# Kernel tuning notes

Hardware: AMD Instinct MI355X
Metric: run time of the kernel (lower is better)

The kernel has to match this reference:

```python
import jax, jax.numpy as jnp
import numpy as np

EPS = 1e-5
C_M, C, C_Z = 256, 32, 128
N_SEQ, N_RES = 256, 1024


def setup_inputs() -> dict:
    key = jax.random.key(0)
    k1, k2, k3 = jax.random.split(key, 3)
    msa = jax.random.normal(k1, (N_SEQ, N_RES, C_M), dtype=jnp.float32)
    norm_w = jnp.ones((C_M,), dtype=jnp.float32)
    norm_b = jnp.zeros((C_M,), dtype=jnp.float32)
    w_ab = jax.random.normal(k2, (C, C_M), dtype=jnp.float32) * (1.0 / np.sqrt(C_M))
    b_ab = jnp.zeros((C,), dtype=jnp.float32)
    w_out = jax.random.normal(k3, (C_Z, C * C), dtype=jnp.float32) * (1.0 / C)
    b_out = jnp.zeros((C_Z,), dtype=jnp.float32)
    return {"msa": msa, "norm_w": norm_w, "norm_b": norm_b,
            "w_ab": w_ab, "b_ab": b_ab, "w_out": w_out, "b_out": b_out}


def reference(msa, norm_w, norm_b, w_ab, b_ab, w_out, b_out):
    # msa: (s, r, c_m) -> (r, s, c_m)
    x = jnp.transpose(msa, (1, 0, 2))
    s = x.shape[1]
    # LayerNorm over c_m
    mu = jnp.mean(x, axis=-1, keepdims=True)
    var = jnp.mean(jnp.square(x - mu), axis=-1, keepdims=True)
    xn = (x - mu) * jax.lax.rsqrt(var + EPS) * norm_w + norm_b
    # a == b: same linear applied twice to same input in the original
    a = jnp.einsum('rsm,cm->rsc', xn, w_ab) + b_ab          # (r, s, c)
    # mean over s of outer product == batched A^T A / s  -> (r, c, c)
    o = jnp.einsum('rsx,rsy->rxy', a, a) / s
    o = o.reshape(o.shape[0], C * C)                        # (r, c*c)
    pre_pair = jnp.einsum('rk,zk->rz', o, w_out) + b_out    # (r, c_z)
    r = pre_pair.shape[0]
    # unsqueeze(1).expand(r, r, c_z)
    pair = jnp.broadcast_to(pre_pair[:, None, :], (r, r, C_Z))
    return pair
```

## Files before the change

kernel.cpp:

```cpp
#include <hip/hip_runtime.h>

#define NSEQ 256
#define NRES 1024
#define CM   256
#define CC   32
#define CZ   128
#define EPS  1e-5f
#define SROW (NRES * CM)
#define MCH  32
#define XPAD 36

typedef float f4v __attribute__((ext_vector_type(4)));

__global__ void opm_setup(const float* __restrict__ nw,
                          const float* __restrict__ nb,
                          const float* __restrict__ w_ab,
                          const float* __restrict__ b_ab,
                          float* __restrict__ wt_g,
                          float* __restrict__ k12)
{
    __shared__ float wls[CM * CC];
    const int t = threadIdx.x;
    const float nwm = nw[t];
    #pragma unroll
    for (int c = 0; c < CC; ++c)
        wls[t * CC + c] = nwm * w_ab[c * CM + t];
    __syncthreads();
    for (int i = t; i < CM * CC; i += 256) wt_g[i] = wls[i];
    if (t < CC) {
        float k1 = 0.f, k2 = 0.f;
        for (int m = 0; m < CM; ++m) {
            k1 += wls[m * CC + t];
            k2 = fmaf(nb[m], w_ab[t * CM + m], k2);
        }
        k12[t]      = k1;
        k12[CC + t] = k2 + b_ab[t];
    }
}

__launch_bounds__(256, 3)
__global__ void opm_compute(const float* __restrict__ msa,
                            const float* __restrict__ wt_g,
                            const float* __restrict__ k12,
                            const float* __restrict__ w_out,
                            const float* __restrict__ b_out,
                            float* __restrict__ pre_out)
{
    __shared__ float xt[NSEQ * XPAD];
    __shared__ float o_lds[CC * CC];
    __shared__ float mu_s[NSEQ];
    __shared__ float rs_s[NSEQ];
    __shared__ float pre_part[2 * CZ];

    const int tid  = threadIdx.x;
    const int r    = blockIdx.x;
    const int lane = tid & 63;
    const int wave = tid >> 6;
    const int cw   = __builtin_amdgcn_readfirstlane(wave << 3);

    const int sc = tid & 7;
    const int sg = tid >> 3;
    const float* xr = msa + (size_t)r * CM;

    float G[4][8];
    #pragma unroll
    for (int j = 0; j < 4; ++j)
        #pragma unroll
        for (int c = 0; c < 8; ++c) G[j][c] = 0.f;

    float psum[8], pssq[8];
    #pragma unroll
    for (int k = 0; k < 8; ++k) { psum[k] = 0.f; pssq[k] = 0.f; }

    float4 pf[8];
    #pragma unroll
    for (int k = 0; k < 8; ++k)
        pf[k] = *(const float4*)(xr + (size_t)(sg + (k << 5)) * SROW + (sc << 2));

    for (int mb = 0; mb < CM; mb += MCH) {
        __syncthreads();
        #pragma unroll
        for (int k = 0; k < 8; ++k) {
            *(float4*)&xt[(sg + (k << 5)) * XPAD + (sc << 2)] = pf[k];
            psum[k] += (pf[k].x + pf[k].y) + (pf[k].z + pf[k].w);
            pssq[k]  = fmaf(pf[k].x, pf[k].x, fmaf(pf[k].y, pf[k].y,
                       fmaf(pf[k].z, pf[k].z, fmaf(pf[k].w, pf[k].w, pssq[k]))));
        }
        __syncthreads();
        if (mb + MCH < CM) {
            #pragma unroll
            for (int k = 0; k < 8; ++k)
                pf[k] = *(const float4*)(xr + (size_t)(sg + (k << 5)) * SROW + (mb + MCH) + (sc << 2));
        }
        #pragma unroll
        for (int mm = 0; mm < MCH; mm += 4) {
            const float4 x0 = *(const float4*)&xt[(lane      ) * XPAD + mm];
            const float4 x1 = *(const float4*)&xt[(lane +  64) * XPAD + mm];
            const float4 x2 = *(const float4*)&xt[(lane + 128) * XPAD + mm];
            const float4 x3 = *(const float4*)&xt[(lane + 192) * XPAD + mm];
            const float* wr = wt_g + (((mb + mm) << 5) + cw);
            #pragma unroll
            for (int kk = 0; kk < 4; ++kk) {
                float wv[8];
                #pragma unroll
                for (int c = 0; c < 8; ++c) wv[c] = wr[(kk << 5) + c];
                const float a0 = (kk == 0) ? x0.x : (kk == 1) ? x0.y : (kk == 2) ? x0.z : x0.w;
                const float a1 = (kk == 0) ? x1.x : (kk == 1) ? x1.y : (kk == 2) ? x1.z : x1.w;
                const float a2 = (kk == 0) ? x2.x : (kk == 1) ? x2.y : (kk == 2) ? x2.z : x2.w;
                const float a3 = (kk == 0) ? x3.x : (kk == 1) ? x3.y : (kk == 2) ? x3.z : x3.w;
                #pragma unroll
                for (int c = 0; c < 8; ++c) {
                    G[0][c] = fmaf(a0, wv[c], G[0][c]);
                    G[1][c] = fmaf(a1, wv[c], G[1][c]);
                    G[2][c] = fmaf(a2, wv[c], G[2][c]);
                    G[3][c] = fmaf(a3, wv[c], G[3][c]);
                }
            }
        }
    }

    #pragma unroll
    for (int k = 0; k < 8; ++k) {
        float s1 = psum[k], s2 = pssq[k];
        s1 += __shfl_xor(s1, 1); s1 += __shfl_xor(s1, 2); s1 += __shfl_xor(s1, 4);
        s2 += __shfl_xor(s2, 1); s2 += __shfl_xor(s2, 2); s2 += __shfl_xor(s2, 4);
        if (sc == 0) {
            const float mu  = s1 * (1.f / CM);
            const float var = s2 * (1.f / CM) - mu * mu;
            mu_s[sg + (k << 5)] = mu;
            rs_s[sg + (k << 5)] = 1.f / sqrtf(var + EPS);
        }
    }
    __syncthreads();

    {
        float k1v[8], k2v[8];
        #pragma unroll
        for (int c = 0; c < 8; ++c) { k1v[c] = k12[cw + c]; k2v[c] = k12[CC + cw + c]; }
        #pragma unroll
        for (int j = 0; j < 4; ++j) {
            const int s = lane + (j << 6);
            const float mu = mu_s[s], rstd = rs_s[s];
            float av[8];
            #pragma unroll
            for (int c = 0; c < 8; ++c)
                av[c] = fmaf(rstd, G[j][c] - mu * k1v[c], k2v[c]);
            const int sw = s & 7;
            *(float4*)&xt[s * CC + ((((wave << 1)    ) ^ sw) << 2)] =
                make_float4(av[0], av[1], av[2], av[3]);
            *(float4*)&xt[s * CC + ((((wave << 1) | 1) ^ sw) << 2)] =
                make_float4(av[4], av[5], av[6], av[7]);
        }
    }
    __syncthreads();

    const int grp = wave;
    const int xs  = (tid >> 3) & 7;
    const int ys  = tid & 7;
    float4 pr0 = {0,0,0,0}, pr1 = {0,0,0,0}, pr2 = {0,0,0,0}, pr3 = {0,0,0,0};
    #pragma unroll 4
    for (int si = 0; si < 64; ++si) {
        const int s  = (grp << 6) + si;
        const int sw = si & 7;
        const float4 ax = *(const float4*)&xt[s * CC + ((xs ^ sw) << 2)];
        const float4 ay = *(const float4*)&xt[s * CC + ((ys ^ sw) << 2)];
        pr0.x = fmaf(ax.x, ay.x, pr0.x); pr0.y = fmaf(ax.x, ay.y, pr0.y);
        pr0.z = fmaf(ax.x, ay.z, pr0.z); pr0.w = fmaf(ax.x, ay.w, pr0.w);
        pr1.x = fmaf(ax.y, ay.x, pr1.x); pr1.y = fmaf(ax.y, ay.y, pr1.y);
        pr1.z = fmaf(ax.y, ay.z, pr1.z); pr1.w = fmaf(ax.y, ay.w, pr1.w);
        pr2.x = fmaf(ax.z, ay.x, pr2.x); pr2.y = fmaf(ax.z, ay.y, pr2.y);
        pr2.z = fmaf(ax.z, ay.z, pr2.z); pr2.w = fmaf(ax.z, ay.w, pr2.w);
        pr3.x = fmaf(ax.w, ay.x, pr3.x); pr3.y = fmaf(ax.w, ay.y, pr3.y);
        pr3.z = fmaf(ax.w, ay.z, pr3.z); pr3.w = fmaf(ax.w, ay.w, pr3.w);
    }
    __syncthreads();
    {
        float* pb = &xt[(grp << 10) + ((xs << 2) * CC) + (ys << 2)];
        *(float4*)&pb[0 * CC] = pr0;
        *(float4*)&pb[1 * CC] = pr1;
        *(float4*)&pb[2 * CC] = pr2;
        *(float4*)&pb[3 * CC] = pr3;
    }
    __syncthreads();
    {
        const float inv_s = 1.f / NSEQ;
        float4 acc = *(const float4*)&xt[(tid << 2)];
        const float4 b1 = *(const float4*)&xt[1024 + (tid << 2)];
        const float4 b2 = *(const float4*)&xt[2048 + (tid << 2)];
        const float4 b3 = *(const float4*)&xt[3072 + (tid << 2)];
        acc.x = (acc.x + b1.x + b2.x + b3.x) * inv_s;
        acc.y = (acc.y + b1.y + b2.y + b3.y) * inv_s;
        acc.z = (acc.z + b1.z + b2.z + b3.z) * inv_s;
        acc.w = (acc.w + b1.w + b2.w + b3.w) * inv_s;
        *(float4*)&o_lds[tid << 2] = acc;
    }
    __syncthreads();

    {
        const int z    = tid & 127;
        const int half = tid >> 7;
        const float* wrow = w_out + (size_t)z * (CC * CC) + half * 512;
        const float* op   = o_lds + half * 512;
        float po = 0.f;
        #pragma unroll 8
        for (int k = 0; k < 512; k += 4) {
            const float4 o4 = *(const float4*)&op[k];
            const float4 w4 = *(const float4*)&wrow[k];
            po = fmaf(o4.x, w4.x, fmaf(o4.y, w4.y, fmaf(o4.z, w4.z, fmaf(o4.w, w4.w, po))));
        }
        pre_part[half * CZ + z] = po;
    }
    __syncthreads();
    if (tid < CZ)
        pre_out[(size_t)r * CZ + tid] = pre_part[tid] + pre_part[CZ + tid] + b_out[tid];
}

__launch_bounds__(256, 8)
__global__ void opm_bcast(const float* __restrict__ pre,
                          float* __restrict__ out)
{
    const int bid = blockIdx.x;
    const int r   = bid >> 3;
    const int jb  = bid & 7;
    const int z4  = threadIdx.x & 31;
    const int jo  = threadIdx.x >> 5;

    const f4v pv = *((const f4v*)(pre + (size_t)r * CZ) + z4);
    f4v* outp = (f4v*)out + ((size_t)r * NRES + (size_t)jb * 128) * (CZ / 4);
    for (int j0 = 0; j0 < 128; j0 += 8)
        __builtin_nontemporal_store(pv, &outp[(size_t)(j0 + jo) * (CZ / 4) + z4]);
}

extern "C" void kernel_launch(void* const* d_in, const int* in_sizes, int n_in,
                              void* d_out, int out_size, void* d_ws, size_t ws_size,
                              hipStream_t stream) {
    const float* msa   = (const float*)d_in[0];
    const float* nw    = (const float*)d_in[1];
    const float* nb    = (const float*)d_in[2];
    const float* w_ab  = (const float*)d_in[3];
    const float* b_ab  = (const float*)d_in[4];
    const float* w_out = (const float*)d_in[5];
    const float* b_out = (const float*)d_in[6];
    float* out = (float*)d_out;

    float* pre  = (float*)d_ws;
    float* wt_g = pre + (size_t)NRES * CZ;
    float* k12  = wt_g + CM * CC;

    opm_setup<<<1, 256, 0, stream>>>(nw, nb, w_ab, b_ab, wt_g, k12);
    opm_compute<<<NRES, 256, 0, stream>>>(msa, wt_g, k12, w_out, b_out, pre);
    opm_bcast<<<NRES * 8, 256, 0, stream>>>(pre, out);
}
```

Measured before the change: 822.2 us.

## Stage projection weights in LDS and remap per-thread tile for LN-projection GEMM

The folded projection weights are copied once per block into shared memory instead of being read from global memory inside the inner loop. The thread tile changes from 4 sequences by 8 channels to 8 sequences by 4 channels, with float4 weight loads from LDS. The msa staging chunk shrinks from 32 to 16 columns, and the smaller buffers are aliased into the existing arrays to keep LDS usage down. The trade-off is 32KB of extra LDS per block, which may lower occupancy, and twice as many chunk iterations and barriers.

```diff
diff --git a/kernel.cpp b/kernel.cpp
--- a/kernel.cpp
+++ b/kernel.cpp
@@ -7,8 +7,8 @@
 #define CZ   128
 #define EPS  1e-5f
 #define SROW (NRES * CM)
-#define MCH  32
-#define XPAD 36
+#define MCH  16
+#define XPAD 20
 
 typedef float f4v __attribute__((ext_vector_type(4)));
 
@@ -46,42 +46,46 @@
                             const float* __restrict__ b_out,
                             float* __restrict__ pre_out)
 {
+    __shared__ float wt[CM * CC];
     __shared__ float xt[NSEQ * XPAD];
-    __shared__ float o_lds[CC * CC];
-    __shared__ float mu_s[NSEQ];
-    __shared__ float rs_s[NSEQ];
-    __shared__ float pre_part[2 * CZ];
 
     const int tid  = threadIdx.x;
     const int r    = blockIdx.x;
-    const int lane = tid & 63;
     const int wave = tid >> 6;
-    const int cw   = __builtin_amdgcn_readfirstlane(wave << 3);
-
-    const int sc = tid & 7;
-    const int sg = tid >> 3;
+
+    const int sc4 = tid & 3;
+    const int sg4 = tid >> 2;
+    const int sc8 = tid & 7;
+    const int sg8 = tid >> 3;
+    const int c0  = sc8 << 2;
+
     const float* xr = msa + (size_t)r * CM;
 
-    float G[4][8];
-    #pragma unroll
-    for (int j = 0; j < 4; ++j)
-        #pragma unroll
-        for (int c = 0; c < 8; ++c) G[j][c] = 0.f;
-
-    float psum[8], pssq[8];
-    #pragma unroll
-    for (int k = 0; k < 8; ++k) { psum[k] = 0.f; pssq[k] = 0.f; }
-
-    float4 pf[8];
-    #pragma unroll
-    for (int k = 0; k < 8; ++k)
-        pf[k] = *(const float4*)(xr + (size_t)(sg + (k << 5)) * SROW + (sc << 2));
+    float4 pf[4];
+    #pragma unroll
+    for (int k = 0; k < 4; ++k)
+        pf[k] = *(const float4*)(xr + (size_t)(sg4 + (k << 6)) * SROW + (sc4 << 2));
+
+    #pragma unroll
+    for (int k = 0; k < 8; ++k) {
+        const int i = (tid + (k << 8)) << 2;
+        *(float4*)&wt[i] = *(const float4*)&wt_g[i];
+    }
+
+    float G[8][4];
+    #pragma unroll
+    for (int j = 0; j < 8; ++j) {
+        G[j][0] = 0.f; G[j][1] = 0.f; G[j][2] = 0.f; G[j][3] = 0.f;
+    }
+    float psum[4], pssq[4];
+    #pragma unroll
+    for (int k = 0; k < 4; ++k) { psum[k] = 0.f; pssq[k] = 0.f; }
 
     for (int mb = 0; mb < CM; mb += MCH) {
         __syncthreads();
         #pragma unroll
-        for (int k = 0; k < 8; ++k) {
-            *(float4*)&xt[(sg + (k << 5)) * XPAD + (sc << 2)] = pf[k];
+        for (int k = 0; k < 4; ++k) {
+            *(float4*)&xt[(sg4 + (k << 6)) * XPAD + (sc4 << 2)] = pf[k];
             psum[k] += (pf[k].x + pf[k].y) + (pf[k].z + pf[k].w);
             pssq[k]  = fmaf(pf[k].x, pf[k].x, fmaf(pf[k].y, pf[k].y,
                        fmaf(pf[k].z, pf[k].z, fmaf(pf[k].w, pf[k].w, pssq[k]))));
@@ -89,67 +93,55 @@
         __syncthreads();
         if (mb + MCH < CM) {
             #pragma unroll
-            for (int k = 0; k < 8; ++k)
-                pf[k] = *(const float4*)(xr + (size_t)(sg + (k << 5)) * SROW + (mb + MCH) + (sc << 2));
+            for (int k = 0; k < 4; ++k)
+                pf[k] = *(const float4*)(xr + (size_t)(sg4 + (k << 6)) * SROW + (mb + MCH) + (sc4 << 2));
         }
         #pragma unroll
         for (int mm = 0; mm < MCH; mm += 4) {
-            const float4 x0 = *(const float4*)&xt[(lane      ) * XPAD + mm];
-            const float4 x1 = *(const float4*)&xt[(lane +  64) * XPAD + mm];
-            const float4 x2 = *(const float4*)&xt[(lane + 128) * XPAD + mm];
-            const float4 x3 = *(const float4*)&xt[(lane + 192) * XPAD + mm];
-            const float* wr = wt_g + (((mb + mm) << 5) + cw);
+            const float4 w0 = *(const float4*)&wt[(mb + mm + 0) * CC + c0];
+            const float4 w1 = *(const float4*)&wt[(mb + mm + 1) * CC + c0];
+            const float4 w2 = *(const float4*)&wt[(mb + mm + 2) * CC + c0];
+            const float4 w3 = *(const float4*)&wt[(mb + mm + 3) * CC + c0];
             #pragma unroll
-            for (int kk = 0; kk < 4; ++kk) {
-                float wv[8];
-                #pragma unroll
-                for (int c = 0; c < 8; ++c) wv[c] = wr[(kk << 5) + c];
-                const float a0 = (kk == 0) ? x0.x : (kk == 1) ? x0.y : (kk == 2) ? x0.z : x0.w;
-                const float a1 = (kk == 0) ? x1.x : (kk == 1) ? x1.y : (kk == 2) ? x1.z : x1.w;
-                const float a2 = (kk == 0) ? x2.x : (kk == 1) ? x2.y : (kk == 2) ? x2.z : x2.w;
-                const float a3 = (kk == 0) ? x3.x : (kk == 1) ? x3.y : (kk == 2) ? x3.z : x3.w;
-                #pragma unroll
-                for (int c = 0; c < 8; ++c) {
-                    G[0][c] = fmaf(a0, wv[c], G[0][c]);
-                    G[1][c] = fmaf(a1, wv[c], G[1][c]);
-                    G[2][c] = fmaf(a2, wv[c], G[2][c]);
-                    G[3][c] = fmaf(a3, wv[c], G[3][c]);
-                }
+            for (int j = 0; j < 8; ++j) {
+                const float4 x4 = *(const float4*)&xt[(sg8 + (j << 5)) * XPAD + mm];
+                G[j][0] = fmaf(x4.x, w0.x, fmaf(x4.y, w1.x, fmaf(x4.z, w2.x, fmaf(x4.w, w3.x, G[j][0]))));
+                G[j][1] = fmaf(x4.x, w0.y, fmaf(x4.y, w1.y, fmaf(x4.z, w2.y, fmaf(x4.w, w3.y, G[j][1]))));
+                G[j][2] = fmaf(x4.x, w0.z, fmaf(x4.y, w1.z, fmaf(x4.z, w2.z, fmaf(x4.w, w3.z, G[j][2]))));
+                G[j][3] = fmaf(x4.x, w0.w, fmaf(x4.y, w1.w, fmaf(x4.z, w2.w, fmaf(x4.w, w3.w, G[j][3]))));
             }
         }
     }
-
-    #pragma unroll
-    for (int k = 0; k < 8; ++k) {
+    __syncthreads();
+
+    #pragma unroll
+    for (int k = 0; k < 4; ++k) {
         float s1 = psum[k], s2 = pssq[k];
-        s1 += __shfl_xor(s1, 1); s1 += __shfl_xor(s1, 2); s1 += __shfl_xor(s1, 4);
-        s2 += __shfl_xor(s2, 1); s2 += __shfl_xor(s2, 2); s2 += __shfl_xor(s2, 4);
-        if (sc == 0) {
+        s1 += __shfl_xor(s1, 1); s1 += __shfl_xor(s1, 2);
+        s2 += __shfl_xor(s2, 1); s2 += __shfl_xor(s2, 2);
+        if (sc4 == 0) {
+            const int s = sg4 + (k << 6);
             const float mu  = s1 * (1.f / CM);
             const float var = s2 * (1.f / CM) - mu * mu;
-            mu_s[sg + (k << 5)] = mu;
-            rs_s[sg + (k << 5)] = 1.f / sqrtf(var + EPS);
-        }
-    }
-    __syncthreads();
-
-    {
-        float k1v[8], k2v[8];
+            xt[s]        = mu;
+            xt[NSEQ + s] = 1.f / sqrtf(var + EPS);
+        }
+    }
+    __syncthreads();
+
+    {
+        const float4 k1v = *(const float4*)&k12[c0];
+        const float4 k2v = *(const float4*)&k12[CC + c0];
         #pragma unroll
-        for (int c = 0; c < 8; ++c) { k1v[c] = k12[cw + c]; k2v[c] = k12[CC + cw + c]; }
-        #pragma unroll
-        for (int j = 0; j < 4; ++j) {
-            const int s = lane + (j << 6);
-            const float mu = mu_s[s], rstd = rs_s[s];
-            float av[8];
-            #pragma unroll
-            for (int c = 0; c < 8; ++c)
-                av[c] = fmaf(rstd, G[j][c] - mu * k1v[c], k2v[c]);
-            const int sw = s & 7;
-            *(float4*)&xt[s * CC + ((((wave << 1)    ) ^ sw) << 2)] =
-                make_float4(av[0], av[1], av[2], av[3]);
-            *(float4*)&xt[s * CC + ((((wave << 1) | 1) ^ sw) << 2)] =
-                make_float4(av[4], av[5], av[6], av[7]);
+        for (int j = 0; j < 8; ++j) {
+            const int s = sg8 + (j << 5);
+            const float mu = xt[s], rstd = xt[NSEQ + s];
+            float4 av;
+            av.x = fmaf(rstd, G[j][0] - mu * k1v.x, k2v.x);
+            av.y = fmaf(rstd, G[j][1] - mu * k1v.y, k2v.y);
+            av.z = fmaf(rstd, G[j][2] - mu * k1v.z, k2v.z);
+            av.w = fmaf(rstd, G[j][3] - mu * k1v.w, k2v.w);
+            *(float4*)&wt[s * CC + ((sc8 ^ (s & 7)) << 2)] = av;
         }
     }
     __syncthreads();
@@ -162,8 +154,8 @@
     for (int si = 0; si < 64; ++si) {
         const int s  = (grp << 6) + si;
         const int sw = si & 7;
-        const float4 ax = *(const float4*)&xt[s * CC + ((xs ^ sw) << 2)];
-        const float4 ay = *(const float4*)&xt[s * CC + ((ys ^ sw) << 2)];
+        const float4 ax = *(const float4*)&wt[s * CC + ((xs ^ sw) << 2)];
+        const float4 ay = *(const float4*)&wt[s * CC + ((ys ^ sw) << 2)];
         pr0.x = fmaf(ax.x, ay.x, pr0.x); pr0.y = fmaf(ax.x, ay.y, pr0.y);
         pr0.z = fmaf(ax.x, ay.z, pr0.z); pr0.w = fmaf(ax.x, ay.w, pr0.w);
         pr1.x = fmaf(ax.y, ay.x, pr1.x); pr1.y = fmaf(ax.y, ay.y, pr1.y);
@@ -173,13 +165,12 @@
         pr3.x = fmaf(ax.w, ay.x, pr3.x); pr3.y = fmaf(ax.w, ay.y, pr3.y);
         pr3.z = fmaf(ax.w, ay.z, pr3.z); pr3.w = fmaf(ax.w, ay.w, pr3.w);
     }
-    __syncthreads();
-    {
-        float* pb = &xt[(grp << 10) + ((xs << 2) * CC) + (ys << 2)];
-        *(float4*)&pb[0 * CC] = pr0;
-        *(float4*)&pb[1 * CC] = pr1;
-        *(float4*)&pb[2 * CC] = pr2;
-        *(float4*)&pb[3 * CC] = pr3;
+    {
+        float* pb = &xt[(grp << 10) + (xs << 7) + (ys << 2)];
+        *(float4*)&pb[0 << 5] = pr0;
+        *(float4*)&pb[1 << 5] = pr1;
+        *(float4*)&pb[2 << 5] = pr2;
+        *(float4*)&pb[3 << 5] = pr3;
     }
     __syncthreads();
     {
@@ -192,7 +183,7 @@
         acc.y = (acc.y + b1.y + b2.y + b3.y) * inv_s;
         acc.z = (acc.z + b1.z + b2.z + b3.z) * inv_s;
         acc.w = (acc.w + b1.w + b2.w + b3.w) * inv_s;
-        *(float4*)&o_lds[tid << 2] = acc;
+        *(float4*)&xt[tid << 2] = acc;
     }
     __syncthreads();
 
@@ -200,7 +191,7 @@
         const int z    = tid & 127;
         const int half = tid >> 7;
         const float* wrow = w_out + (size_t)z * (CC * CC) + half * 512;
-        const float* op   = o_lds + half * 512;
+        const float* op   = &xt[half * 512];
         float po = 0.f;
         #pragma unroll 8
         for (int k = 0; k < 512; k += 4) {
@@ -208,11 +199,11 @@
             const float4 w4 = *(const float4*)&wrow[k];
             po = fmaf(o4.x, w4.x, fmaf(o4.y, w4.y, fmaf(o4.z, w4.z, fmaf(o4.w, w4.w, po))));
         }
-        pre_part[half * CZ + z] = po;
+        xt[4096 + (half << 7) + z] = po;
     }
     __syncthreads();
     if (tid < CZ)
-        pre_out[(size_t)r * CZ + tid] = pre_part[tid] + pre_part[CZ + tid] + b_out[tid];
+        pre_out[(size_t)r * CZ + tid] = xt[4096 + tid] + xt[4096 + CZ + tid] + b_out[tid];
 }
 
 __launch_bounds__(256, 8)
```

After: 795.4 us. 1.03x faster.

## Use split-bf16 MFMA for LayerNorm-projection GEMM instead of scalar FP32 FMAs

Applied to the files above, without the earlier changes.

Replaces the scalar FP32 FMA loop computing x·W (256 seq × 256 ch × 32 out per residue) with bf16 MFMA 16x16x32 instructions. Precision is kept by splitting both x and W into high and low bf16 parts and summing three cross products. Weights are pre-split and pre-swizzled into MFMA fragment layout in the setup kernel and staged in LDS. LDS use grows, so launch bounds drop to 2 blocks per CU. The approach risks small numerical error from dropping the low×low term.

```diff
diff --git a/kernel.cpp b/kernel.cpp
--- a/kernel.cpp
+++ b/kernel.cpp
@@ -7,17 +7,25 @@
 #define CZ   128
 #define EPS  1e-5f
 #define SROW (NRES * CM)
-#define MCH  32
-#define XPAD 36
 
 typedef float f4v __attribute__((ext_vector_type(4)));
+typedef __attribute__((ext_vector_type(8))) short short8;
+typedef __attribute__((ext_vector_type(4))) float f32x4;
+typedef unsigned int u32;
+
+__device__ __forceinline__ float trunc_bf16(float f) {
+    return __uint_as_float(__float_as_uint(f) & 0xffff0000u);
+}
+__device__ __forceinline__ u32 pk_bf16(float a, float b) {
+    return (__float_as_uint(b) & 0xffff0000u) | (__float_as_uint(a) >> 16);
+}
 
 __global__ void opm_setup(const float* __restrict__ nw,
                           const float* __restrict__ nb,
                           const float* __restrict__ w_ab,
                           const float* __restrict__ b_ab,
-                          float* __restrict__ wt_g,
-                          float* __restrict__ k12)
+                          float* __restrict__ k12,
+                          unsigned short* __restrict__ wb_su)
 {
     __shared__ float wls[CM * CC];
     const int t = threadIdx.x;
@@ -26,7 +34,6 @@
     for (int c = 0; c < CC; ++c)
         wls[t * CC + c] = nwm * w_ab[c * CM + t];
     __syncthreads();
-    for (int i = t; i < CM * CC; i += 256) wt_g[i] = wls[i];
     if (t < CC) {
         float k1 = 0.f, k2 = 0.f;
         for (int m = 0; m < CM; ++m) {
@@ -36,38 +43,54 @@
         k12[t]      = k1;
         k12[CC + t] = k2 + b_ab[t];
     }
-}
-
-__launch_bounds__(256, 3)
+    for (int e = t; e < 16384; e += 256) {
+        const int j     = e & 7;
+        const int l     = (e >> 3) & 63;
+        const int split = (e >> 9) & 1;
+        const int nt    = (e >> 10) & 1;
+        const int kk    = e >> 11;
+        const int m = (kk << 5) + ((l >> 4) << 3) + j;
+        const int c = (nt << 4) + (l & 15);
+        const float w  = wls[m * CC + c];
+        const float w1 = trunc_bf16(w);
+        const float v  = split ? (w - w1) : w;
+        wb_su[e] = (unsigned short)(__float_as_uint(v) >> 16);
+    }
+}
+
+__launch_bounds__(256, 2)
 __global__ void opm_compute(const float* __restrict__ msa,
-                            const float* __restrict__ wt_g,
+                            const u32*  __restrict__ wb_g,
                             const float* __restrict__ k12,
                             const float* __restrict__ w_out,
                             const float* __restrict__ b_out,
                             float* __restrict__ pre_out)
 {
-    __shared__ float xt[NSEQ * XPAD];
-    __shared__ float o_lds[CC * CC];
-    __shared__ float mu_s[NSEQ];
-    __shared__ float rs_s[NSEQ];
-    __shared__ float pre_part[2 * CZ];
-
-    const int tid  = threadIdx.x;
-    const int r    = blockIdx.x;
-    const int lane = tid & 63;
-    const int wave = tid >> 6;
-    const int cw   = __builtin_amdgcn_readfirstlane(wave << 3);
-
-    const int sc = tid & 7;
-    const int sg = tid >> 3;
-    const float* xr = msa + (size_t)r * CM;
-
-    float G[4][8];
-    #pragma unroll
-    for (int j = 0; j < 4; ++j)
-        #pragma unroll
-        for (int c = 0; c < 8; ++c) G[j][c] = 0.f;
-
+    __shared__ u32 xp[2 * 5120];
+    __shared__ u32 wbl[8192];
+    __shared__ float st[520];
+
+    const int tid = threadIdx.x;
+    const int r   = blockIdx.x;
+    const int w   = tid >> 6;
+    const int l   = tid & 63;
+
+    const int sc8 = tid & 7;
+    const int sg8 = tid >> 3;
+    const float* xr = msa + (size_t)r * CM + (sc8 << 2);
+
+    u32* xp1 = xp;
+    u32* xp2 = xp + 5120;
+
+    #pragma unroll
+    for (int k = 0; k < 8; ++k) {
+        const int i = (tid + (k << 8)) << 2;
+        *(f4v*)&wbl[i] = *(const f4v*)&wb_g[i];
+    }
+
+    f32x4 acc[4][2];
+    #pragma unroll
+    for (int mt = 0; mt < 4; ++mt) { acc[mt][0] = (f32x4)0.f; acc[mt][1] = (f32x4)0.f; }
     float psum[8], pssq[8];
     #pragma unroll
     for (int k = 0; k < 8; ++k) { psum[k] = 0.f; pssq[k] = 0.f; }
@@ -75,95 +98,101 @@
     float4 pf[8];
     #pragma unroll
     for (int k = 0; k < 8; ++k)
-        pf[k] = *(const float4*)(xr + (size_t)(sg + (k << 5)) * SROW + (sc << 2));
-
-    for (int mb = 0; mb < CM; mb += MCH) {
+        pf[k] = *(const float4*)(xr + (size_t)(sg8 + (k << 5)) * SROW);
+
+    for (int kk = 0; kk < 8; ++kk) {
         __syncthreads();
         #pragma unroll
         for (int k = 0; k < 8; ++k) {
-            *(float4*)&xt[(sg + (k << 5)) * XPAD + (sc << 2)] = pf[k];
-            psum[k] += (pf[k].x + pf[k].y) + (pf[k].z + pf[k].w);
-            pssq[k]  = fmaf(pf[k].x, pf[k].x, fmaf(pf[k].y, pf[k].y,
-                       fmaf(pf[k].z, pf[k].z, fmaf(pf[k].w, pf[k].w, pssq[k]))));
+            const float4 p = pf[k];
+            const int row = sg8 + (k << 5);
+            const u32 a0 = pk_bf16(p.x, p.y), a1 = pk_bf16(p.z, p.w);
+            const float rx = p.x - trunc_bf16(p.x);
+            const float ry = p.y - trunc_bf16(p.y);
+            const float rz = p.z - trunc_bf16(p.z);
+            const float rw = p.w - trunc_bf16(p.w);
+            const u32 b0 = pk_bf16(rx, ry), b1 = pk_bf16(rz, rw);
+            *(uint2*)&xp1[row * 20 + (sc8 << 1)] = make_uint2(a0, a1);
+            *(uint2*)&xp2[row * 20 + (sc8 << 1)] = make_uint2(b0, b1);
+            psum[k] += (p.x + p.y) + (p.z + p.w);
+            pssq[k]  = fmaf(p.x, p.x, fmaf(p.y, p.y, fmaf(p.z, p.z, fmaf(p.w, p.w, pssq[k]))));
         }
         __syncthreads();
-        if (mb + MCH < CM) {
+        if (kk < 7) {
             #pragma unroll
             for (int k = 0; k < 8; ++k)
-                pf[k] = *(const float4*)(xr + (size_t)(sg + (k << 5)) * SROW + (mb + MCH) + (sc << 2));
-        }
-        #pragma unroll
-        for (int mm = 0; mm < MCH; mm += 4) {
-            const float4 x0 = *(const float4*)&xt[(lane      ) * XPAD + mm];
-            const float4 x1 = *(const float4*)&xt[(lane +  64) * XPAD + mm];
-            const float4 x2 = *(const float4*)&xt[(lane + 128) * XPAD + mm];
-            const float4 x3 = *(const float4*)&xt[(lane + 192) * XPAD + mm];
-            const float* wr = wt_g + (((mb + mm) << 5) + cw);
+                pf[k] = *(const float4*)(xr + (size_t)(sg8 + (k << 5)) * SROW + ((kk + 1) << 5));
+        }
+        short8 B[2][2];
+        #pragma unroll
+        for (int nt = 0; nt < 2; ++nt)
             #pragma unroll
-            for (int kk = 0; kk < 4; ++kk) {
-                float wv[8];
-                #pragma unroll
-                for (int c = 0; c < 8; ++c) wv[c] = wr[(kk << 5) + c];
-                const float a0 = (kk == 0) ? x0.x : (kk == 1) ? x0.y : (kk == 2) ? x0.z : x0.w;
-                const float a1 = (kk == 0) ? x1.x : (kk == 1) ? x1.y : (kk == 2) ? x1.z : x1.w;
-                const float a2 = (kk == 0) ? x2.x : (kk == 1) ? x2.y : (kk == 2) ? x2.z : x2.w;
-                const float a3 = (kk == 0) ? x3.x : (kk == 1) ? x3.y : (kk == 2) ? x3.z : x3.w;
-                #pragma unroll
-                for (int c = 0; c < 8; ++c) {
-                    G[0][c] = fmaf(a0, wv[c], G[0][c]);
-                    G[1][c] = fmaf(a1, wv[c], G[1][c]);
-                    G[2][c] = fmaf(a2, wv[c], G[2][c]);
-                    G[3][c] = fmaf(a3, wv[c], G[3][c]);
-                }
+            for (int sp = 0; sp < 2; ++sp) {
+                const int fb = ((((kk << 1) + nt) << 1) + sp) * 256 + (l << 2);
+                B[nt][sp] = __builtin_bit_cast(short8, *(const f4v*)&wbl[fb]);
             }
-        }
-    }
+        #pragma unroll
+        for (int mt = 0; mt < 4; ++mt) {
+            const int arow = ((w << 6) + (mt << 4) + (l & 15)) * 20 + ((l >> 4) << 2);
+            const short8 A1 = __builtin_bit_cast(short8, *(const f4v*)&xp1[arow]);
+            const short8 A2 = __builtin_bit_cast(short8, *(const f4v*)&xp2[arow]);
+            acc[mt][0] = __builtin_amdgcn_mfma_f32_16x16x32_bf16(A1, B[0][0], acc[mt][0], 0, 0, 0);
+            acc[mt][1] = __builtin_amdgcn_mfma_f32_16x16x32_bf16(A1, B[1][0], acc[mt][1], 0, 0, 0);
+            acc[mt][0] = __builtin_amdgcn_mfma_f32_16x16x32_bf16(A1, B[0][1], acc[mt][0], 0, 0, 0);
+            acc[mt][1] = __builtin_amdgcn_mfma_f32_16x16x32_bf16(A1, B[1][1], acc[mt][1], 0, 0, 0);
+            acc[mt][0] = __builtin_amdgcn_mfma_f32_16x16x32_bf16(A2, B[0][0], acc[mt][0], 0, 0, 0);
+            acc[mt][1] = __builtin_amdgcn_mfma_f32_16x16x32_bf16(A2, B[1][0], acc[mt][1], 0, 0, 0);
+        }
+    }
+    __syncthreads();
 
     #pragma unroll
     for (int k = 0; k < 8; ++k) {
         float s1 = psum[k], s2 = pssq[k];
         s1 += __shfl_xor(s1, 1); s1 += __shfl_xor(s1, 2); s1 += __shfl_xor(s1, 4);
         s2 += __shfl_xor(s2, 1); s2 += __shfl_xor(s2, 2); s2 += __shfl_xor(s2, 4);
-        if (sc == 0) {
+        if (sc8 == 0) {
+            const int s = sg8 + (k << 5);
             const float mu  = s1 * (1.f / CM);
             const float var = s2 * (1.f / CM) - mu * mu;
-            mu_s[sg + (k << 5)] = mu;
-            rs_s[sg + (k << 5)] = 1.f / sqrtf(var + EPS);
-        }
-    }
-    __syncthreads();
-
-    {
-        float k1v[8], k2v[8];
-        #pragma unroll
-        for (int c = 0; c < 8; ++c) { k1v[c] = k12[cw + c]; k2v[c] = k12[CC + cw + c]; }
-        #pragma unroll
-        for (int j = 0; j < 4; ++j) {
-            const int s = lane + (j << 6);
-            const float mu = mu_s[s], rstd = rs_s[s];
-            float av[8];
+            st[s]        = mu;
+            st[256 + s]  = 1.f / sqrtf(var + EPS);
+        }
+    }
+    __syncthreads();
+
+    float* aB = (float*)xp;
+    {
+        const int cl = l & 15;
+        const float k1_0 = k12[cl],      k1_1 = k12[16 + cl];
+        const float k2_0 = k12[CC + cl], k2_1 = k12[CC + 16 + cl];
+        #pragma unroll
+        for (int mt = 0; mt < 4; ++mt) {
             #pragma unroll
-            for (int c = 0; c < 8; ++c)
-                av[c] = fmaf(rstd, G[j][c] - mu * k1v[c], k2v[c]);
-            const int sw = s & 7;
-            *(float4*)&xt[s * CC + ((((wave << 1)    ) ^ sw) << 2)] =
-                make_float4(av[0], av[1], av[2], av[3]);
-            *(float4*)&xt[s * CC + ((((wave << 1) | 1) ^ sw) << 2)] =
-                make_float4(av[4], av[5], av[6], av[7]);
-        }
-    }
-    __syncthreads();
-
-    const int grp = wave;
-    const int xs  = (tid >> 3) & 7;
-    const int ys  = tid & 7;
+            for (int rg = 0; rg < 4; ++rg) {
+                const int s = (w << 6) + (mt << 4) + ((l >> 4) << 2) + rg;
+                const float mu = st[s], rs = st[256 + s];
+                const float a0 = fmaf(rs, acc[mt][0][rg] - mu * k1_0, k2_0);
+                const float a1 = fmaf(rs, acc[mt][1][rg] - mu * k1_1, k2_1);
+                const int sw = s & 7;
+                aB[s * CC + (((cl >> 2) ^ sw) << 2) + (cl & 3)]       = a0;
+                aB[s * CC + ((((cl >> 2) + 4) ^ sw) << 2) + (cl & 3)] = a1;
+            }
+        }
+    }
+    __syncthreads();
+
+    float* scr = (float*)wbl;
+    const int grp = w;
+    const int xs_ = (tid >> 3) & 7;
+    const int ys_ = tid & 7;
     float4 pr0 = {0,0,0,0}, pr1 = {0,0,0,0}, pr2 = {0,0,0,0}, pr3 = {0,0,0,0};
     #pragma unroll 4
     for (int si = 0; si < 64; ++si) {
         const int s  = (grp << 6) + si;
-        const int sw = si & 7;
-        const float4 ax = *(const float4*)&xt[s * CC + ((xs ^ sw) << 2)];
-        const float4 ay = *(const float4*)&xt[s * CC + ((ys ^ sw) << 2)];
+        const int sw = s & 7;
+        const float4 ax = *(const float4*)&aB[s * CC + ((xs_ ^ sw) << 2)];
+        const float4 ay = *(const float4*)&aB[s * CC + ((ys_ ^ sw) << 2)];
         pr0.x = fmaf(ax.x, ay.x, pr0.x); pr0.y = fmaf(ax.x, ay.y, pr0.y);
         pr0.z = fmaf(ax.x, ay.z, pr0.z); pr0.w = fmaf(ax.x, ay.w, pr0.w);
         pr1.x = fmaf(ax.y, ay.x, pr1.x); pr1.y = fmaf(ax.y, ay.y, pr1.y);
@@ -173,9 +202,8 @@
         pr3.x = fmaf(ax.w, ay.x, pr3.x); pr3.y = fmaf(ax.w, ay.y, pr3.y);
         pr3.z = fmaf(ax.w, ay.z, pr3.z); pr3.w = fmaf(ax.w, ay.w, pr3.w);
     }
-    __syncthreads();
-    {
-        float* pb = &xt[(grp << 10) + ((xs << 2) * CC) + (ys << 2)];
+    {
+        float* pb = &scr[(grp << 10) + ((xs_ << 2) * CC) + (ys_ << 2)];
         *(float4*)&pb[0 * CC] = pr0;
         *(float4*)&pb[1 * CC] = pr1;
         *(float4*)&pb[2 * CC] = pr2;
@@ -184,15 +212,15 @@
     __syncthreads();
     {
         const float inv_s = 1.f / NSEQ;
-        float4 acc = *(const float4*)&xt[(tid << 2)];
-        const float4 b1 = *(const float4*)&xt[1024 + (tid << 2)];
-        const float4 b2 = *(const float4*)&xt[2048 + (tid << 2)];
-        const float4 b3 = *(const float4*)&xt[3072 + (tid << 2)];
-        acc.x = (acc.x + b1.x + b2.x + b3.x) * inv_s;
-        acc.y = (acc.y + b1.y + b2.y + b3.y) * inv_s;
-        acc.z = (acc.z + b1.z + b2.z + b3.z) * inv_s;
-        acc.w = (acc.w + b1.w + b2.w + b3.w) * inv_s;
-        *(float4*)&o_lds[tid << 2] = acc;
+        float4 a4 = *(const float4*)&scr[(tid << 2)];
+        const float4 b1 = *(const float4*)&scr[1024 + (tid << 2)];
+        const float4 b2 = *(const float4*)&scr[2048 + (tid << 2)];
+        const float4 b3 = *(const float4*)&scr[3072 + (tid << 2)];
+        a4.x = (a4.x + b1.x + b2.x + b3.x) * inv_s;
+        a4.y = (a4.y + b1.y + b2.y + b3.y) * inv_s;
+        a4.z = (a4.z + b1.z + b2.z + b3.z) * inv_s;
+        a4.w = (a4.w + b1.w + b2.w + b3.w) * inv_s;
+        *(float4*)&scr[tid << 2] = a4;
     }
     __syncthreads();
 
@@ -200,7 +228,7 @@
         const int z    = tid & 127;
         const int half = tid >> 7;
         const float* wrow = w_out + (size_t)z * (CC * CC) + half * 512;
-        const float* op   = o_lds + half * 512;
+        const float* op   = &scr[half * 512];
         float po = 0.f;
         #pragma unroll 8
         for (int k = 0; k < 512; k += 4) {
@@ -208,11 +236,11 @@
             const float4 w4 = *(const float4*)&wrow[k];
             po = fmaf(o4.x, w4.x, fmaf(o4.y, w4.y, fmaf(o4.z, w4.z, fmaf(o4.w, w4.w, po))));
         }
-        pre_part[half * CZ + z] = po;
+        scr[4096 + (half << 7) + z] = po;
     }
     __syncthreads();
     if (tid < CZ)
-        pre_out[(size_t)r * CZ + tid] = pre_part[tid] + pre_part[CZ + tid] + b_out[tid];
+        pre_out[(size_t)r * CZ + tid] = scr[4096 + tid] + scr[4096 + CZ + tid] + b_out[tid];
 }
 
 __launch_bounds__(256, 8)
@@ -243,11 +271,11 @@
     const float* b_out = (const float*)d_in[6];
     float* out = (float*)d_out;
 
-    float* pre  = (float*)d_ws;
-    float* wt_g = pre + (size_t)NRES * CZ;
-    float* k12  = wt_g + CM * CC;
-
-    opm_setup<<<1, 256, 0, stream>>>(nw, nb, w_ab, b_ab, wt_g, k12);
-    opm_compute<<<NRES, 256, 0, stream>>>(msa, wt_g, k12, w_out, b_out, pre);
+    float* pre = (float*)d_ws;
+    float* k12 = pre + (size_t)NRES * CZ;
+    unsigned short* wb_su = (unsigned short*)(k12 + 64);
+
+    opm_setup<<<1, 256, 0, stream>>>(nw, nb, w_ab, b_ab, k12, wb_su);
+    opm_compute<<<NRES, 256, 0, stream>>>(msa, (const u32*)wb_su, k12, w_out, b_out, pre);
     opm_bcast<<<NRES * 8, 256, 0, stream>>>(pre, out);
 }
```

New measurement: 791.4 us. -3.7%, faster.
